# Optimization experiments

Hardware: AMD Instinct MI355X
Metric: run time of the kernel (lower is better)

The kernel has to match this reference:

```python
import jax, jax.numpy as jnp
import numpy as np

B, H, L, T, D = 2, 12, 1024, 1024, 64
FEA = 3
DIM = H * D  # 768


def setup_inputs() -> dict:
    key = jax.random.key(0)
    ks = jax.random.split(key, 8)
    return {
        "s0": jax.random.normal(ks[0], (B, H, L, T), jnp.float32),
        "s1": jax.random.normal(ks[1], (B, H, L, T), jnp.float32),
        "s2": jax.random.normal(ks[2], (B, H, L, T), jnp.float32),
        "v": jax.random.normal(ks[3], (B, H, T, D), jnp.float32),
        "fuse_w": jax.random.normal(ks[4], (H, H * FEA), jnp.float32) * 0.1,
        "fuse_b": jax.random.normal(ks[5], (H,), jnp.float32) * 0.1,
        "proj_w": jax.random.normal(ks[6], (DIM, DIM), jnp.float32) * 0.02,
        "proj_b": jax.random.normal(ks[7], (DIM,), jnp.float32) * 0.02,
    }


def reference(s0, s1, s2, v, fuse_w, fuse_b, proj_w, proj_b):
    # concat score maps along channel dim: [b, h*fea, l, t]
    scores = jnp.concatenate([s0, s1, s2], axis=1)
    # 1x1 conv fusion over channel dim: [b, h, l, t]
    fused = jnp.einsum('bclt,oc->bolt', scores, fuse_w) + fuse_b[None, :, None, None]
    # softmax over keys (last dim)
    attn = jax.nn.softmax(fused, axis=-1)
    # attn @ V: [b, h, l, d]
    x = jnp.einsum('bhlt,bhtd->bhld', attn, v)
    # merge heads: [b, l, h*d]
    b, h, l, d = x.shape
    x = jnp.transpose(x, (0, 2, 1, 3)).reshape(b, l, h * d)
    # output projection (torch Linear: x @ W.T + b)
    return x @ proj_w.T + proj_b
```

## Files before the change

### kernel.cpp

```cpp
#include <hip/hip_runtime.h>
#include <hip/hip_bf16.h>

typedef __attribute__((ext_vector_type(8))) short short8;
typedef __attribute__((ext_vector_type(8))) unsigned short ushort8;
typedef __attribute__((ext_vector_type(4))) float f32x4;

#define NB 2
#define NH 12
#define NL 1024
#define NT 1024
#define ND 64
#define NCH 36
#define DIM 768

static __device__ __forceinline__ unsigned short f2bf(float x) {
  union { float f; unsigned int u; } c; c.f = x;
  unsigned int r = c.u + 0x7fffu + ((c.u >> 16) & 1u);
  return (unsigned short)(r >> 16);
}

__global__ __launch_bounds__(256) void k_fuse_softmax(
    const float* __restrict__ s0, const float* __restrict__ s1,
    const float* __restrict__ s2, const float* __restrict__ fw,
    unsigned short* __restrict__ attn)
{
  __shared__ float wS[NCH][NH];
  __shared__ float fused[NH][NT];
  const int tid = threadIdx.x;
  const int b = blockIdx.x >> 10;
  const int l = blockIdx.x & 1023;

  for (int i = tid; i < NCH * NH; i += 256) {
    int h = i % NH, c = i / NH;
    wS[c][h] = fw[h * NCH + c];
  }
  __syncthreads();

  float acc[NH][4];
#pragma unroll
  for (int h = 0; h < NH; ++h) {
    acc[h][0] = 0.f; acc[h][1] = 0.f; acc[h][2] = 0.f; acc[h][3] = 0.f;
  }

  const int t0 = tid * 4;
  const size_t base = (size_t)b * NH * NL * NT + (size_t)l * NT + t0;
  const float* sp0 = s0 + base;
  const float* sp1 = s1 + base;
  const float* sp2 = s2 + base;
#pragma unroll
  for (int g = 0; g < 3; ++g) {
    const float* p = (g == 0) ? sp0 : (g == 1) ? sp1 : sp2;
#pragma unroll
    for (int ch = 0; ch < NH; ++ch) {
      float4 sv = *(const float4*)(p + (size_t)ch * NL * NT);
#pragma unroll
      for (int h = 0; h < NH; ++h) {
        float w = wS[g * NH + ch][h];
        acc[h][0] = fmaf(w, sv.x, acc[h][0]);
        acc[h][1] = fmaf(w, sv.y, acc[h][1]);
        acc[h][2] = fmaf(w, sv.z, acc[h][2]);
        acc[h][3] = fmaf(w, sv.w, acc[h][3]);
      }
    }
  }
#pragma unroll
  for (int h = 0; h < NH; ++h) {
    *(float4*)&fused[h][t0] = make_float4(acc[h][0], acc[h][1], acc[h][2], acc[h][3]);
  }
  __syncthreads();

  const int wv = tid >> 6, lane = tid & 63;
  for (int i = 0; i < 3; ++i) {
    const int h = wv * 3 + i;
    float v[16];
    float m = -3.0e38f;
#pragma unroll
    for (int k = 0; k < 16; ++k) {
      v[k] = fused[h][lane + 64 * k];
      m = fmaxf(m, v[k]);
    }
#pragma unroll
    for (int off = 32; off > 0; off >>= 1) m = fmaxf(m, __shfl_xor(m, off));
    float s = 0.f;
#pragma unroll
    for (int k = 0; k < 16; ++k) { v[k] = __expf(v[k] - m); s += v[k]; }
#pragma unroll
    for (int off = 32; off > 0; off >>= 1) s += __shfl_xor(s, off);
    const float inv = 1.0f / s;
    unsigned short* op = attn + ((size_t)(b * NH + h) * NL + l) * NT;
#pragma unroll
    for (int k = 0; k < 16; ++k) op[lane + 64 * k] = f2bf(v[k] * inv);
  }
}

__global__ __launch_bounds__(256) void k_transpose_v(
    const float* __restrict__ v, unsigned short* __restrict__ vT)
{
  __shared__ float vS[128][65];
  const int tid = threadIdx.x;
  const int tt = blockIdx.x;
  const int h = blockIdx.y, b = blockIdx.z;
  const int t0 = tt * 128;
  const float* vp = v + ((size_t)(b * NH + h) * NT + t0) * ND;
#pragma unroll
  for (int r = 0; r < 8; ++r) {
    int f = tid + r * 256;
    int t = f >> 4, d4 = (f & 15) * 4;
    float4 x = *(const float4*)(vp + (size_t)t * ND + d4);
    vS[t][d4 + 0] = x.x; vS[t][d4 + 1] = x.y;
    vS[t][d4 + 2] = x.z; vS[t][d4 + 3] = x.w;
  }
  __syncthreads();
  unsigned short* op = vT + (size_t)(b * NH + h) * ND * NT;
#pragma unroll
  for (int r = 0; r < 4; ++r) {
    int c = tid + r * 256;
    int d = c >> 4, tl = (c & 15) * 8;
    ushort8 u;
#pragma unroll
    for (int j = 0; j < 8; ++j) u[j] = f2bf(vS[tl + j][d]);
    *(ushort8*)(op + (size_t)d * NT + t0 + tl) = u;
  }
}

__global__ __launch_bounds__(128) void k_pv(
    const unsigned short* __restrict__ attn,
    const unsigned short* __restrict__ vT,
    unsigned short* __restrict__ xb)
{
  __shared__ unsigned short vS[64][136];
  const int tid = threadIdx.x;
  const int lane = tid & 63, wv = tid >> 6;
  const int lt = blockIdx.x, h = blockIdx.y, b = blockIdx.z;
  const int l0 = lt * 32;
  const unsigned short* ap = attn + ((size_t)(b * NH + h) * NL + l0) * NT;
  const unsigned short* vp = vT + (size_t)(b * NH + h) * ND * NT;
  f32x4 acc[4] = {};
  const int arow = wv * 16 + (lane & 15);
  const int kg = (lane >> 4) * 8;
  const int bn = lane & 15;

  for (int kt = 0; kt < 8; ++kt) {
    __syncthreads();
#pragma unroll
    for (int r = 0; r < 8; ++r) {
      int c = tid + r * 128;
      int d = c >> 4, tl = (c & 15) * 8;
      *(ushort8*)&vS[d][tl] = *(const ushort8*)(vp + (size_t)d * NT + kt * 128 + tl);
    }
    __syncthreads();
#pragma unroll
    for (int ks = 0; ks < 4; ++ks) {
      short8 af = *(const short8*)(ap + (size_t)arow * NT + kt * 128 + ks * 32 + kg);
#pragma unroll
      for (int dt = 0; dt < 4; ++dt) {
        short8 bf = *(const short8*)&vS[dt * 16 + bn][ks * 32 + kg];
        acc[dt] = __builtin_amdgcn_mfma_f32_16x16x32_bf16(af, bf, acc[dt], 0, 0, 0);
      }
    }
  }
  const int crow0 = wv * 16 + (lane >> 4) * 4;
#pragma unroll
  for (int dt = 0; dt < 4; ++dt) {
#pragma unroll
    for (int r = 0; r < 4; ++r) {
      int row = l0 + crow0 + r;
      xb[((size_t)b * NL + row) * DIM + h * ND + dt * 16 + bn] = f2bf(acc[dt][r]);
    }
  }
}

__global__ __launch_bounds__(256) void k_proj(
    const unsigned short* __restrict__ xb, const float* __restrict__ pw,
    const float* __restrict__ pb, float* __restrict__ out)
{
  __shared__ unsigned short wS[64][136];
  const int tid = threadIdx.x;
  const int lane = tid & 63, wv = tid >> 6;
  const int n0 = blockIdx.x * 64, o0 = blockIdx.y * 64;
  f32x4 acc[4] = {};
  const int kg = (lane >> 4) * 8;
  const int bn = lane & 15;
  const int arow = n0 + wv * 16 + bn;

  for (int kt = 0; kt < 6; ++kt) {
    __syncthreads();
#pragma unroll
    for (int r = 0; r < 4; ++r) {
      int c = tid + r * 256;
      int oi = c >> 4, kl = (c & 15) * 8;
      const float* wp = pw + (size_t)(o0 + oi) * DIM + kt * 128 + kl;
      float4 x0 = *(const float4*)(wp);
      float4 x1 = *(const float4*)(wp + 4);
      ushort8 u;
      u[0] = f2bf(x0.x); u[1] = f2bf(x0.y); u[2] = f2bf(x0.z); u[3] = f2bf(x0.w);
      u[4] = f2bf(x1.x); u[5] = f2bf(x1.y); u[6] = f2bf(x1.z); u[7] = f2bf(x1.w);
      *(ushort8*)&wS[oi][kl] = u;
    }
    __syncthreads();
#pragma unroll
    for (int ks = 0; ks < 4; ++ks) {
      short8 af = *(const short8*)(xb + (size_t)arow * DIM + kt * 128 + ks * 32 + kg);
#pragma unroll
      for (int ot = 0; ot < 4; ++ot) {
        short8 bf = *(const short8*)&wS[ot * 16 + bn][ks * 32 + kg];
        acc[ot] = __builtin_amdgcn_mfma_f32_16x16x32_bf16(af, bf, acc[ot], 0, 0, 0);
      }
    }
  }
  const int crow0 = wv * 16 + (lane >> 4) * 4;
#pragma unroll
  for (int ot = 0; ot < 4; ++ot) {
    const int oc = o0 + ot * 16 + bn;
    const float bias = pb[oc];
#pragma unroll
    for (int r = 0; r < 4; ++r) {
      int row = n0 + crow0 + r;
      out[(size_t)row * DIM + oc] = acc[ot][r] + bias;
    }
  }
}

extern "C" void kernel_launch(void* const* d_in, const int* in_sizes, int n_in,
                              void* d_out, int out_size, void* d_ws, size_t ws_size,
                              hipStream_t stream) {
  const float* s0 = (const float*)d_in[0];
  const float* s1 = (const float*)d_in[1];
  const float* s2 = (const float*)d_in[2];
  const float* v  = (const float*)d_in[3];
  const float* fw = (const float*)d_in[4];
  const float* pw = (const float*)d_in[6];
  const float* pb = (const float*)d_in[7];
  float* out = (float*)d_out;

  const size_t attn_bytes = (size_t)NB * NH * NL * NT * 2;
  const size_t vT_bytes   = (size_t)NB * NH * ND * NT * 2;
  unsigned short* attn = (unsigned short*)d_ws;
  unsigned short* vT   = (unsigned short*)((char*)d_ws + attn_bytes);
  unsigned short* xb   = (unsigned short*)((char*)d_ws + attn_bytes + vT_bytes);

  k_fuse_softmax<<<dim3(NB * NL), dim3(256), 0, stream>>>(s0, s1, s2, fw, attn);
  k_transpose_v<<<dim3(8, NH, NB), dim3(256), 0, stream>>>(v, vT);
  k_pv<<<dim3(32, NH, NB), dim3(128), 0, stream>>>(attn, vT, xb);
  k_proj<<<dim3(32, DIM / 64), dim3(256), 0, stream>>>(xb, pw, pb, out);
}
```

Baseline: 126.4 us.

## Compute softmax in registers with cross-wave reductions instead of shared staging

The fuse+softmax kernel no longer stages the 12x1024 fused scores in shared memory. Each thread keeps its 4 columns for all 12 heads in registers and computes the max and sum through wave shuffles plus a small shared reduction buffer across the four waves. The bf16 output is written as 4-element vector stores instead of scalar 2-byte stores, and the fusion weights are read as float4 rows. It also sets a minimum-occupancy launch bound of 4 blocks per CU, which adds register pressure from the 12 per-head shuffle reductions but removes 48KB of LDS per block.

```diff
diff --git a/kernel.cpp b/kernel.cpp
--- a/kernel.cpp
+++ b/kernel.cpp
@@ -3,6 +3,7 @@
 
 typedef __attribute__((ext_vector_type(8))) short short8;
 typedef __attribute__((ext_vector_type(8))) unsigned short ushort8;
+typedef __attribute__((ext_vector_type(4))) unsigned short u16x4;
 typedef __attribute__((ext_vector_type(4))) float f32x4;
 
 #define NB 2
@@ -19,16 +20,17 @@
   return (unsigned short)(r >> 16);
 }
 
-__global__ __launch_bounds__(256) void k_fuse_softmax(
+__global__ __launch_bounds__(256, 4) void k_fuse_softmax(
     const float* __restrict__ s0, const float* __restrict__ s1,
     const float* __restrict__ s2, const float* __restrict__ fw,
     unsigned short* __restrict__ attn)
 {
-  __shared__ float wS[NCH][NH];
-  __shared__ float fused[NH][NT];
+  __shared__ float wS[NCH][16];
+  __shared__ float red[2][4][NH];
   const int tid = threadIdx.x;
   const int b = blockIdx.x >> 10;
   const int l = blockIdx.x & 1023;
+  const int wv = tid >> 6, lane = tid & 63;
 
   for (int i = tid; i < NCH * NH; i += 256) {
     int h = i % NH, c = i / NH;
@@ -44,52 +46,73 @@
 
   const int t0 = tid * 4;
   const size_t base = (size_t)b * NH * NL * NT + (size_t)l * NT + t0;
-  const float* sp0 = s0 + base;
-  const float* sp1 = s1 + base;
-  const float* sp2 = s2 + base;
+  const float* ps[3] = { s0 + base, s1 + base, s2 + base };
 #pragma unroll
   for (int g = 0; g < 3; ++g) {
-    const float* p = (g == 0) ? sp0 : (g == 1) ? sp1 : sp2;
+    const float* p = ps[g];
 #pragma unroll
     for (int ch = 0; ch < NH; ++ch) {
       float4 sv = *(const float4*)(p + (size_t)ch * NL * NT);
+      float wreg[NH];
+      *(float4*)&wreg[0] = *(const float4*)&wS[g * NH + ch][0];
+      *(float4*)&wreg[4] = *(const float4*)&wS[g * NH + ch][4];
+      *(float4*)&wreg[8] = *(const float4*)&wS[g * NH + ch][8];
 #pragma unroll
       for (int h = 0; h < NH; ++h) {
-        float w = wS[g * NH + ch][h];
-        acc[h][0] = fmaf(w, sv.x, acc[h][0]);
-        acc[h][1] = fmaf(w, sv.y, acc[h][1]);
-        acc[h][2] = fmaf(w, sv.z, acc[h][2]);
-        acc[h][3] = fmaf(w, sv.w, acc[h][3]);
+        acc[h][0] = fmaf(wreg[h], sv.x, acc[h][0]);
+        acc[h][1] = fmaf(wreg[h], sv.y, acc[h][1]);
+        acc[h][2] = fmaf(wreg[h], sv.z, acc[h][2]);
+        acc[h][3] = fmaf(wreg[h], sv.w, acc[h][3]);
       }
     }
   }
-#pragma unroll
-  for (int h = 0; h < NH; ++h) {
-    *(float4*)&fused[h][t0] = make_float4(acc[h][0], acc[h][1], acc[h][2], acc[h][3]);
-  }
-  __syncthreads();
-
-  const int wv = tid >> 6, lane = tid & 63;
-  for (int i = 0; i < 3; ++i) {
-    const int h = wv * 3 + i;
-    float v[16];
-    float m = -3.0e38f;
-#pragma unroll
-    for (int k = 0; k < 16; ++k) {
-      v[k] = fused[h][lane + 64 * k];
-      m = fmaxf(m, v[k]);
-    }
-#pragma unroll
-    for (int off = 32; off > 0; off >>= 1) m = fmaxf(m, __shfl_xor(m, off));
-    float s = 0.f;
-#pragma unroll
-    for (int k = 0; k < 16; ++k) { v[k] = __expf(v[k] - m); s += v[k]; }
-#pragma unroll
-    for (int off = 32; off > 0; off >>= 1) s += __shfl_xor(s, off);
-    const float inv = 1.0f / s;
-    unsigned short* op = attn + ((size_t)(b * NH + h) * NL + l) * NT;
-#pragma unroll
-    for (int k = 0; k < 16; ++k) op[lane + 64 * k] = f2bf(v[k] * inv);
+
+  float mx[NH];
+#pragma unroll
+  for (int h = 0; h < NH; ++h) {
+    mx[h] = fmaxf(fmaxf(acc[h][0], acc[h][1]), fmaxf(acc[h][2], acc[h][3]));
+#pragma unroll
+    for (int off = 32; off > 0; off >>= 1)
+      mx[h] = fmaxf(mx[h], __shfl_xor(mx[h], off));
+  }
+  if (lane == 0) {
+#pragma unroll
+    for (int h = 0; h < NH; ++h) red[0][wv][h] = mx[h];
+  }
+  __syncthreads();
+#pragma unroll
+  for (int h = 0; h < NH; ++h)
+    mx[h] = fmaxf(fmaxf(red[0][0][h], red[0][1][h]),
+                  fmaxf(red[0][2][h], red[0][3][h]));
+
+  float sm[NH];
+#pragma unroll
+  for (int h = 0; h < NH; ++h) {
+    acc[h][0] = __expf(acc[h][0] - mx[h]);
+    acc[h][1] = __expf(acc[h][1] - mx[h]);
+    acc[h][2] = __expf(acc[h][2] - mx[h]);
+    acc[h][3] = __expf(acc[h][3] - mx[h]);
+    sm[h] = (acc[h][0] + acc[h][1]) + (acc[h][2] + acc[h][3]);
+#pragma unroll
+    for (int off = 32; off > 0; off >>= 1)
+      sm[h] += __shfl_xor(sm[h], off);
+  }
+  if (lane == 0) {
+#pragma unroll
+    for (int h = 0; h < NH; ++h) red[1][wv][h] = sm[h];
+  }
+  __syncthreads();
+
+#pragma unroll
+  for (int h = 0; h < NH; ++h) {
+    float s = (red[1][0][h] + red[1][1][h]) + (red[1][2][h] + red[1][3][h]);
+    float inv = 1.0f / s;
+    u16x4 u;
+    u[0] = f2bf(acc[h][0] * inv);
+    u[1] = f2bf(acc[h][1] * inv);
+    u[2] = f2bf(acc[h][2] * inv);
+    u[3] = f2bf(acc[h][3] * inv);
+    *(u16x4*)(attn + ((size_t)(b * NH + h) * NL + l) * NT + t0) = u;
   }
 }
 
```

New measurement: 114.3 us. 9.6% less time.
